# Optimization experiments

Measured on AMD Instinct MI355X. Metric: run time of the kernel, lower is better.

The kernel has to match this reference:

```python
import jax, jax.numpy as jnp
import numpy as np
from jax import lax

# 2D MPS-RNN (one-site, hilbert_local=2, real params, snake order, 'regular' phase)
# Faithful reconstruction of MPS_RNN_2D forward: site-by-site recurrence over an
# L x M lattice. At each site: candidate hidden states for both local occupations
#   h_cand[s] = M_h[i,j,s] @ h_left + M_v[i,j,s] @ h_below + v[i,j,s]
# conditional prob p(s) ~ sum_d eta[i,j,d]^2 * h_cand[s,d]^2 (eta-weighted norm),
# selected hidden state is renormalized; phase accumulates arg(w.h + c) (0 or pi
# for real params). Returns [B,2]: (log|psi|, phase).

L, M, S, D = 8, 8, 2, 32   # rows, cols, local Hilbert dim, bond dim dcut
B = 32768                  # batch of sampled configurations
NQ = L * M                 # nqubits
EPS = 1e-10


def setup_inputs() -> dict:
    key = jax.random.key(0)
    ks = jax.random.split(key, 7)
    sc = np.float32(1.0 / np.sqrt(D))  # keep hidden-state norms O(1)
    x = jax.random.randint(ks[0], (B, NQ), 0, 2, dtype=jnp.int32)
    M_h = jax.random.normal(ks[1], (L, M, S, D, D), jnp.float32) * sc
    M_v = jax.random.normal(ks[2], (L, M, S, D, D), jnp.float32) * sc
    v = jax.random.normal(ks[3], (L, M, S, D), jnp.float32) * sc
    w = jax.random.normal(ks[4], (L, M, D), jnp.float32) * sc
    c = jnp.zeros((L, M), jnp.float32)
    eta = jax.random.normal(ks[5], (L, M, D), jnp.float32)
    return {"x": x, "M_h": M_h, "M_v": M_v, "v": v, "w": w, "c": c, "eta": eta}


def _forward(x, M_h, M_v, v, w, c, eta):
    dt = M_h.dtype
    # snake order: odd rows are scanned right-to-left in lattice coordinates.
    cols = jnp.arange(M)
    odd = (jnp.arange(L) % 2 == 1)[:, None]
    colmap = jnp.where(odd, M - 1 - cols[None, :], cols[None, :])  # [L,M] scan-pos -> lattice col (involution)
    ri = jnp.arange(L)[:, None]
    gather = lambda p: p[ri, colmap]  # reorder params into scan order per row
    M_h_s, M_v_s, v_s, w_s, c_s, eta_s = (gather(p) for p in (M_h, M_v, v, w, c, eta))
    x_s = x.reshape(B, L, M).transpose(1, 2, 0)  # [L,M,B] already in qubit/scan order

    pi_f = jnp.asarray(np.pi, dt)

    def col_step(h_h, cin):
        Mh, Mv, vv, ww, cc, ee, xx, hv = cin
        # candidate states for both local occupations: [B,S,D]
        hc = (jnp.einsum('sab,Bb->Bsa', Mh, h_h)
              + jnp.einsum('sab,Bb->Bsa', Mv, hv)
              + vv[None])
        p = jnp.einsum('Bsa,a->Bs', hc * hc, ee * ee)  # eta-weighted squared norms
        psel = jnp.take_along_axis(p, xx[:, None], axis=1)[:, 0]
        dla = 0.5 * (jnp.log(psel + EPS) - jnp.log(p.sum(-1) + EPS))
        hsel = jnp.take_along_axis(hc, xx[:, None, None], axis=1)[:, 0]  # [B,D]
        hn = hsel / (jnp.sqrt(jnp.sum(hsel * hsel, -1, keepdims=True)) + EPS)
        a = hn @ ww + cc  # [B]
        dph = jnp.where(a < 0, pi_f, jnp.asarray(0, dt))  # arg of real scalar
        return hn, (dla, dph, hn)

    def row_step(carry, rin):
        h_v_lat, la, ph = carry
        Mh_r, Mv_r, v_r, w_r, c_r, e_r, x_r, cmap = rin
        hv_scan = h_v_lat[:, cmap].transpose(1, 0, 2)  # [M,B,D] vertical inputs in scan order
        h0 = jnp.ones((B, D), dt)  # left_boundary = ones
        _, (dlas, dphs, hs) = lax.scan(col_step, h0, (Mh_r, Mv_r, v_r, w_r, c_r, e_r, x_r, hv_scan))
        la = la + dlas.sum(0)
        ph = ph + dphs.sum(0)
        h_new = hs.transpose(1, 0, 2)[:, cmap]  # back to lattice column order (cmap is an involution)
        return (h_new, la, ph), None

    init = (jnp.zeros((B, M, D), dt),  # bottom_boundary = zeros
            jnp.zeros((B,), dt), jnp.zeros((B,), dt))
    (hv, log_amp, phase), _ = lax.scan(row_step, init, (M_h_s, M_v_s, v_s, w_s, c_s, eta_s, x_s, colmap))
    return jnp.stack([log_amp, phase], axis=-1)  # [B,2]


def reference(x, M_h, M_v, v, w, c, eta):
    return _forward(x, M_h, M_v, v, w, c, eta)
```

## Files before the change

kernel.cpp:

```cpp
#include <hip/hip_runtime.h>

#define LROWS 8
#define MCOLS 8
#define BD 32
#define NSITE 64
#define SPB 64
#define BTOT 32768
#define NBLK (BTOT / SPB)
#define EPS 1e-10
#define PI_D 3.14159265358979323846

#define W_OFF 0
#define CB_OFF 262144
#define CC_OFF (262144 + 12288)
#define WS_DBLS (CC_OFF + 64)

__global__ void precompute_kernel(const float* __restrict__ M_h,
                                  const float* __restrict__ M_v,
                                  const float* __restrict__ v,
                                  const float* __restrict__ w,
                                  const float* __restrict__ cc,
                                  const float* __restrict__ eta,
                                  double* __restrict__ ws) {
    int idx = blockIdx.x * 256 + threadIdx.x;
    if (idx >= WS_DBLS) return;
    double val = 0.0;
    if (idx < CB_OFF) {
        int pair = idx & 1, a4 = (idx >> 1) & 3, b = (idx >> 3) & 31;
        int r = (idx >> 8) & 15, site = idx >> 12;
        int i = site >> 3, js = site & 7;
        int c = (i & 1) ? (MCOLS - 1 - js) : js;
        int s = r >> 3, a = (r & 7) * 4 + a4;
        if (pair == 0) val = (double)M_h[(((i * MCOLS + c) * 2 + s) * BD + a) * BD + b];
        else           val = (double)M_v[(((i * MCOLS + c) * 2 + s) * BD + a) * BD + b];
    } else if (idx < CC_OFF) {
        int j = idx - CB_OFF;
        int site = j / 192;
        int rem = j - site * 192;
        int r = rem / 12, t = rem - r * 12;
        int i = site >> 3, js = site & 7;
        int c = (i & 1) ? (MCOLS - 1 - js) : js;
        int s = r >> 3, a0 = (r & 7) * 4;
        if (t < 4)      val = (double)v[(((i * MCOLS + c) * 2 + s) * BD) + a0 + t];
        else if (t < 8) { double e = (double)eta[(i * MCOLS + c) * BD + a0 + (t - 4)]; val = e * e; }
        else            val = (double)w[(i * MCOLS + c) * BD + a0 + (t - 8)];
    } else {
        int site = idx - CC_OFF;
        int i = site >> 3, js = site & 7;
        int c = (i & 1) ? (MCOLS - 1 - js) : js;
        val = (double)cc[i * MCOLS + c];
    }
    ws[idx] = val;
}

__launch_bounds__(1024, 1)
__global__ void mps_main_kernel(const int* __restrict__ x,
                                const double* __restrict__ ws,
                                float* __restrict__ out) {
    __shared__ double hRow[MCOLS][BD][SPB];
    __shared__ float  pbuf[2][16][SPB];
    __shared__ double ssb[16 >> 1][SPB];
    __shared__ double phb[2][8][SPB];

    const int tid = threadIdx.x;
    const int k = tid & 63;
    const int r = tid >> 6;
    const int r_u = __builtin_amdgcn_readfirstlane(r);
    const int s = r_u >> 3;
    const int abase = (r_u & 7) * 4;
    const int j8 = r_u & 7;
    const long kg = (long)blockIdx.x * SPB + k;

    for (int t = tid; t < MCOLS * BD * SPB; t += 1024) (&hRow[0][0][0])[t] = 0.0;
    __syncthreads();

    const double2* __restrict__ Wp = (const double2*)ws;

    double la = 0.0, ph = 0.0;
    double prodN = 1.0, prodD = 1.0;
    int par = 0;
    double2 wreg[2][8];

    {
        const double2* __restrict__ w0 = Wp + (size_t)r_u * 128;
        #pragma unroll
        for (int t = 0; t < 8; ++t) wreg[0][t] = w0[t];
    }

    for (int i = 0; i < LROWS; ++i) {
        const int* xp = x + kg * NSITE + i * MCOLS;
        int4 xa = *reinterpret_cast<const int4*>(xp);
        int4 xb = *reinterpret_cast<const int4*>(xp + 4);
        const unsigned xbits = (unsigned)((xa.x & 1)        | ((xa.y & 1) << 1) |
                                          ((xa.z & 1) << 2) | ((xa.w & 1) << 3) |
                                          ((xb.x & 1) << 4) | ((xb.y & 1) << 5) |
                                          ((xb.z & 1) << 6) | ((xb.w & 1) << 7));
        prodN = 1.0; prodD = 1.0;

        for (int js = 0; js < MCOLS; ++js) {
            const int site = i * MCOLS + js;
            const int c = (i & 1) ? (MCOLS - 1 - js) : js;
            const int cprev = (i & 1) ? (MCOLS - js) : (js - 1);

            const double2* __restrict__ wsite = Wp + (size_t)(site * 16 + r_u) * 128;
            const double*  __restrict__ cb    = ws + CB_OFF + (size_t)(site * 16 + r_u) * 12;

            const double* __restrict__ colV = &hRow[c][0][0];

            double acc[4];
            #pragma unroll
            for (int a = 0; a < 4; ++a) acc[a] = 0.0;

            if (js == 0) {
                #pragma unroll
                for (int bb = 0; bb < 16; ++bb) {
                    const int cur = bb & 1;
                    if (bb < 15) {
                        const double2* __restrict__ wn = wsite + (bb + 1) * 8;
                        #pragma unroll
                        for (int t = 0; t < 8; ++t) wreg[cur ^ 1][t] = wn[t];
                    }
                    #pragma unroll
                    for (int bq = 0; bq < 2; ++bq) {
                        const int b = bb * 2 + bq;
                        const double hvb = colV[b * SPB + k];
                        #pragma unroll
                        for (int a = 0; a < 4; ++a) {
                            const double2 w2 = wreg[cur][bq * 4 + a];
                            acc[a] = fma(w2.y, hvb, acc[a] + w2.x);
                        }
                    }
                }
            } else {
                const double* __restrict__ colL = &hRow[cprev][0][0];
                #pragma unroll
                for (int bb = 0; bb < 16; ++bb) {
                    const int cur = bb & 1;
                    if (bb < 15) {
                        const double2* __restrict__ wn = wsite + (bb + 1) * 8;
                        #pragma unroll
                        for (int t = 0; t < 8; ++t) wreg[cur ^ 1][t] = wn[t];
                    }
                    #pragma unroll
                    for (int bq = 0; bq < 2; ++bq) {
                        const int b = bb * 2 + bq;
                        const double hlb = colL[b * SPB + k];
                        const double hvb = colV[b * SPB + k];
                        #pragma unroll
                        for (int a = 0; a < 4; ++a) {
                            const double2 w2 = wreg[cur][bq * 4 + a];
                            acc[a] = fma(w2.x, hlb, fma(w2.y, hvb, acc[a]));
                        }
                    }
                }
            }
            #pragma unroll
            for (int a = 0; a < 4; ++a) acc[a] += cb[a];

            double pp = 0.0, ssp = 0.0, php = 0.0;
            #pragma unroll
            for (int a = 0; a < 4; ++a) {
                const double t2 = acc[a] * acc[a];
                pp  = fma(t2, cb[4 + a], pp);
                ssp += t2;
                php = fma(acc[a], cb[8 + a], php);
            }
            const double ccoef = ws[CC_OFF + site];
            const int xs = (int)((xbits >> js) & 1u);
            const bool sel = (s == xs);

            pbuf[par][r][k] = (float)pp;
            if (sel) { ssb[j8][k] = ssp; phb[par][j8][k] = php; }
            __syncthreads();

            {
                const double2* __restrict__ wn = Wp + (size_t)((site + 1) * 16 + r_u) * 128;
                #pragma unroll
                for (int t = 0; t < 8; ++t) wreg[0][t] = wn[t];
            }

            const double ss = (((ssb[0][k] + ssb[1][k]) + (ssb[2][k] + ssb[3][k]))
                             + ((ssb[4][k] + ssb[5][k]) + (ssb[6][k] + ssb[7][k])));
            const double inv = 1.0 / (sqrt(ss) + EPS);
            if (sel) {
                #pragma unroll
                for (int a = 0; a < 4; ++a)
                    hRow[c][abase + a][k] = acc[a] * inv;
            }
            __syncthreads();

            if (r_u == 0) {
                const float* __restrict__ pb = &pbuf[par][0][0];
                const double p0 = (double)((((pb[0*SPB+k] + pb[1*SPB+k]) + (pb[2*SPB+k] + pb[3*SPB+k]))
                                          + ((pb[4*SPB+k] + pb[5*SPB+k]) + (pb[6*SPB+k] + pb[7*SPB+k]))));
                const double p1 = (double)((((pb[8*SPB+k] + pb[9*SPB+k]) + (pb[10*SPB+k] + pb[11*SPB+k]))
                                          + ((pb[12*SPB+k] + pb[13*SPB+k]) + (pb[14*SPB+k] + pb[15*SPB+k]))));
                const double psel = xs ? p1 : p0;
                prodN *= (psel + EPS);
                prodD *= (p0 + p1 + EPS);
                const double phd = (((phb[par][0][k] + phb[par][1][k]) + (phb[par][2][k] + phb[par][3][k]))
                                  + ((phb[par][4][k] + phb[par][5][k]) + (phb[par][6][k] + phb[par][7][k])));
                const double aph = phd * inv + ccoef;
                ph += (aph < 0.0) ? PI_D : 0.0;
            }
            par ^= 1;
        }
        if (r_u == 0) la += 0.5 * (log(prodN) - log(prodD));
    }

    if (r == 0) {
        out[kg * 2]     = (float)la;
        out[kg * 2 + 1] = (float)ph;
    }
}

extern "C" void kernel_launch(void* const* d_in, const int* in_sizes, int n_in,
                              void* d_out, int out_size, void* d_ws, size_t ws_size,
                              hipStream_t stream) {
    const int*   x    = (const int*)d_in[0];
    const float* M_h  = (const float*)d_in[1];
    const float* M_v  = (const float*)d_in[2];
    const float* v    = (const float*)d_in[3];
    const float* w    = (const float*)d_in[4];
    const float* cc   = (const float*)d_in[5];
    const float* eta  = (const float*)d_in[6];
    float* out = (float*)d_out;
    double* ws = (double*)d_ws;

    const int pre_total = WS_DBLS;
    dim3 preGrid((pre_total + 255) / 256), preBlock(256);
    hipLaunchKernelGGL(precompute_kernel, preGrid, preBlock, 0, stream,
                       M_h, M_v, v, w, cc, eta, ws);

    dim3 grid(NBLK), block(1024);
    hipLaunchKernelGGL(mps_main_kernel, grid, block, 0, stream, x, ws, out);
}
```

Before: 654.6 us.

## Stream weights contiguously per row-group with a four-deep register prefetch ring

```diff
diff --git a/kernel.cpp b/kernel.cpp
--- a/kernel.cpp
+++ b/kernel.cpp
@@ -27,7 +27,7 @@
     double val = 0.0;
     if (idx < CB_OFF) {
         int pair = idx & 1, a4 = (idx >> 1) & 3, b = (idx >> 3) & 31;
-        int r = (idx >> 8) & 15, site = idx >> 12;
+        int site = (idx >> 8) & 63, r = idx >> 14;
         int i = site >> 3, js = site & 7;
         int c = (i & 1) ? (MCOLS - 1 - js) : js;
         int s = r >> 3, a = (r & 7) * 4 + a4;
@@ -59,7 +59,7 @@
                                 float* __restrict__ out) {
     __shared__ double hRow[MCOLS][BD][SPB];
     __shared__ float  pbuf[2][16][SPB];
-    __shared__ double ssb[16 >> 1][SPB];
+    __shared__ double ssb[8][SPB];
     __shared__ double phb[2][8][SPB];
 
     const int tid = threadIdx.x;
@@ -75,16 +75,18 @@
     __syncthreads();
 
     const double2* __restrict__ Wp = (const double2*)ws;
+    const double2* __restrict__ wstream = Wp + (size_t)r_u * (NSITE * 128);
 
     double la = 0.0, ph = 0.0;
     double prodN = 1.0, prodD = 1.0;
     int par = 0;
-    double2 wreg[2][8];
+    double2 wreg[4][8];
 
     {
-        const double2* __restrict__ w0 = Wp + (size_t)r_u * 128;
         #pragma unroll
-        for (int t = 0; t < 8; ++t) wreg[0][t] = w0[t];
+        for (int cch = 0; cch < 4; ++cch)
+            #pragma unroll
+            for (int t = 0; t < 8; ++t) wreg[cch][t] = wstream[cch * 8 + t];
     }
 
     for (int i = 0; i < LROWS; ++i) {
@@ -102,7 +104,7 @@
             const int c = (i & 1) ? (MCOLS - 1 - js) : js;
             const int cprev = (i & 1) ? (MCOLS - js) : (js - 1);
 
-            const double2* __restrict__ wsite = Wp + (size_t)(site * 16 + r_u) * 128;
+            const double2* __restrict__ wsite = wstream + (size_t)site * 128;
             const double*  __restrict__ cb    = ws + CB_OFF + (size_t)(site * 16 + r_u) * 12;
 
             const double* __restrict__ colV = &hRow[c][0][0];
@@ -114,33 +116,26 @@
             if (js == 0) {
                 #pragma unroll
                 for (int bb = 0; bb < 16; ++bb) {
-                    const int cur = bb & 1;
-                    if (bb < 15) {
-                        const double2* __restrict__ wn = wsite + (bb + 1) * 8;
-                        #pragma unroll
-                        for (int t = 0; t < 8; ++t) wreg[cur ^ 1][t] = wn[t];
-                    }
+                    const int slot = bb & 3;
                     #pragma unroll
                     for (int bq = 0; bq < 2; ++bq) {
                         const int b = bb * 2 + bq;
                         const double hvb = colV[b * SPB + k];
                         #pragma unroll
                         for (int a = 0; a < 4; ++a) {
-                            const double2 w2 = wreg[cur][bq * 4 + a];
+                            const double2 w2 = wreg[slot][bq * 4 + a];
                             acc[a] = fma(w2.y, hvb, acc[a] + w2.x);
                         }
                     }
+                    const double2* __restrict__ wn = wsite + (bb + 4) * 8;
+                    #pragma unroll
+                    for (int t = 0; t < 8; ++t) wreg[slot][t] = wn[t];
                 }
             } else {
                 const double* __restrict__ colL = &hRow[cprev][0][0];
                 #pragma unroll
                 for (int bb = 0; bb < 16; ++bb) {
-                    const int cur = bb & 1;
-                    if (bb < 15) {
-                        const double2* __restrict__ wn = wsite + (bb + 1) * 8;
-                        #pragma unroll
-                        for (int t = 0; t < 8; ++t) wreg[cur ^ 1][t] = wn[t];
-                    }
+                    const int slot = bb & 3;
                     #pragma unroll
                     for (int bq = 0; bq < 2; ++bq) {
                         const int b = bb * 2 + bq;
@@ -148,10 +143,13 @@
                         const double hvb = colV[b * SPB + k];
                         #pragma unroll
                         for (int a = 0; a < 4; ++a) {
-                            const double2 w2 = wreg[cur][bq * 4 + a];
+                            const double2 w2 = wreg[slot][bq * 4 + a];
                             acc[a] = fma(w2.x, hlb, fma(w2.y, hvb, acc[a]));
                         }
                     }
+                    const double2* __restrict__ wn = wsite + (bb + 4) * 8;
+                    #pragma unroll
+                    for (int t = 0; t < 8; ++t) wreg[slot][t] = wn[t];
                 }
             }
             #pragma unroll
@@ -172,12 +170,6 @@
             pbuf[par][r][k] = (float)pp;
             if (sel) { ssb[j8][k] = ssp; phb[par][j8][k] = php; }
             __syncthreads();
-
-            {
-                const double2* __restrict__ wn = Wp + (size_t)((site + 1) * 16 + r_u) * 128;
-                #pragma unroll
-                for (int t = 0; t < 8; ++t) wreg[0][t] = wn[t];
-            }
 
             const double ss = (((ssb[0][k] + ssb[1][k]) + (ssb[2][k] + ssb[3][k]))
                              + ((ssb[4][k] + ssb[5][k]) + (ssb[6][k] + ssb[7][k])));
```

Result: slower. 956.3 us (+46.1%).
